# Kernel optimization log

Measured on AMD Instinct MI355X. Metric: run time of the kernel, lower is better.

Reference implementation:

```python
import jax, jax.numpy as jnp
import numpy as np
import math

B, NS, NT = 8, 512, 512
NSRC, NTRG = B * NS, B * NT
E = 32768
SCALAR_DIM, EMBED, ORI, LAYERS, K, KK = 20, 128, 1024, 3, 5, 25
CONV_IN = 2 * EMBED
FINAL_IN = ORI + LAYERS * EMBED


def sinusoidal_pos_emb(x):
    half = SCALAR_DIM // 2
    freqs = jnp.exp(-(math.log(10000.0) / (half - 1)) * jnp.arange(half, dtype=x.dtype))
    ang = x[:, None] * freqs[None, :]
    return jnp.concatenate([jnp.sin(ang), jnp.cos(ang)], axis=-1)


def spline_basis(pseudo):
    # open B-spline basis, degree 1, kernel_size K per dim, dim=2 (torch_spline_conv semantics)
    v = pseudo * (K - 1)
    lo = jnp.floor(v)
    frac = v - lo
    lo = lo.astype(jnp.int32)
    idxs, ws = [], []
    for s1 in (0, 1):
        for s0 in (0, 1):
            i0 = jnp.clip(lo[:, 0] + s0, 0, K - 1)
            i1 = jnp.clip(lo[:, 1] + s1, 0, K - 1)
            w0 = frac[:, 0] if s0 else 1.0 - frac[:, 0]
            w1 = frac[:, 1] if s1 else 1.0 - frac[:, 1]
            idxs.append(i0 + K * i1)
            ws.append(w0 * w1)
    idx = jnp.stack(idxs, 1)  # [E,4] kernel indices
    w = jnp.stack(ws, 1)      # [E,4] basis weights
    e = pseudo.shape[0]
    # dense [E,KK] coefficient matrix (<=4 nonzeros per row)
    return jnp.zeros((e, KK), pseudo.dtype).at[jnp.arange(e)[:, None], idx].add(w)


def spline_conv(x, edge_index, edge_attr, W, root, bias):
    # SplineConv(in=CONV_IN, out=EMBED, dim=2, kernel_size=5, degree=1, aggr='mean', root_weight=True)
    src, dst = edge_index[0], edge_index[1]
    x_j = x[src]                    # [E, in] gather of source features
    C = spline_basis(edge_attr)     # [E, KK]
    msg = jnp.zeros((x_j.shape[0], W.shape[-1]), x.dtype)
    for k in range(KK):             # fixed small kernel loop (25 GEMMs)
        msg = msg + (C[:, k:k + 1] * x_j) @ W[k]
    n = x.shape[0]
    agg = jax.ops.segment_sum(msg, dst, num_segments=n)
    deg = jax.ops.segment_sum(jnp.ones((msg.shape[0],), x.dtype), dst, num_segments=n)
    agg = agg / jnp.clip(deg, 1.0)[:, None]   # mean aggregation
    return agg + x @ root + bias


def masked_softmax(src, mask):
    out = jnp.where(mask, src, -jnp.inf)
    out = jax.nn.softmax(out, axis=-1)
    return jnp.where(mask, out, 0.0)


def setup_inputs() -> dict:
    key = jax.random.key(0)
    ks = jax.random.split(key, 16)
    s = 0.02
    # block-diagonal edges: both endpoints within the same graph
    gs = jax.random.randint(ks[11], (E,), 0, B)
    gt = jax.random.randint(ks[12], (E,), 0, B)
    ei_s = jnp.stack([gs * NS + jax.random.randint(ks[13], (E,), 0, NS),
                      gs * NS + jax.random.randint(ks[14], (E,), 0, NS)])
    ei_t = jnp.stack([gt * NT + jax.random.randint(ks[15], (E,), 0, NT),
                      gt * NT + jax.random.randint(ks[0], (E,), 0, NT)])
    return {
        "t": jax.random.uniform(ks[1], (B,)),
        "Xt": jax.random.uniform(ks[2], (B, NS, NT)),
        "x_s": jax.random.normal(ks[3], (NSRC, ORI)),
        "x_t": jax.random.normal(ks[4], (NTRG, ORI)),
        "ea_s": jax.random.uniform(ks[5], (E, 2)),
        "ea_t": jax.random.uniform(ks[6], (E, 2)),
        "lin0_w": jax.random.normal(ks[7], (ORI + 2 * SCALAR_DIM, EMBED)) * s,
        "lin0_b": jnp.zeros((EMBED,)),
        "lin_w": jax.random.normal(ks[8], (LAYERS - 1, EMBED + 2 * SCALAR_DIM, EMBED)) * s,
        "lin_b": jnp.zeros((LAYERS - 1, EMBED)),
        "conv_w": jax.random.normal(ks[9], (LAYERS, KK, CONV_IN, EMBED)) * s,
        "conv_root": jax.random.normal(ks[10], (LAYERS, CONV_IN, EMBED)) * s,
        "conv_bias": jnp.zeros((LAYERS, EMBED)),
        "final_w": jax.random.normal(jax.random.fold_in(key, 99), (FINAL_IN, EMBED)) * s,
        "final_b": jnp.zeros((EMBED,)),
        "ei_s": ei_s,
        "ei_t": ei_t,
        "s_mask": jnp.ones((B, NS), dtype=bool),
        "t_mask": jnp.ones((B, NT), dtype=bool),
        "mask_align": jnp.ones((B, NS, NT), dtype=bool),
    }


def reference(t, Xt, x_s, x_t, ea_s, ea_t, lin0_w, lin0_b, lin_w, lin_b,
              conv_w, conv_root, conv_bias, final_w, final_b,
              ei_s, ei_t, s_mask, t_mask, mask_align):
    # All graphs have exactly NS/NT nodes, so s_mask/t_mask are all-True:
    # boolean select x[s_mask] == reshape, and to_dense_batch == reshape.
    time_emb = sinusoidal_pos_emb(t)                                    # [B, 20]
    num_src = sinusoidal_pos_emb(Xt.sum(-1).reshape(-1) / 10.0)         # [NSRC, 20]
    num_trg = sinusoidal_pos_emb(jnp.swapaxes(Xt, 1, 2).sum(-1).reshape(-1) / 10.0)
    tf_src = jnp.repeat(time_emb, NS, axis=0)                           # per-node time features
    tf_trg = jnp.repeat(time_emb, NT, axis=0)
    xs_src, xs_trg = [x_s], [x_t]
    for i in range(LAYERS):
        w = lin0_w if i == 0 else lin_w[i - 1]
        b = lin0_b if i == 0 else lin_b[i - 1]
        xin_s = jnp.concatenate([xs_src[-1], num_src, tf_src], -1) @ w + b
        xin_t = jnp.concatenate([xs_trg[-1], num_trg, tf_trg], -1) @ w + b
        xp_s = xin_s.reshape(B, NS, EMBED)
        xp_t = xin_t.reshape(B, NT, EMBED)
        tgt_msg = jnp.einsum('bst,btd->bsd', Xt, xp_t)
        src_msg = jnp.einsum('bst,bsd->btd', Xt, xp_s)
        diff_s = (xp_s - tgt_msg).reshape(NSRC, EMBED)
        diff_t = (xp_t - src_msg).reshape(NTRG, EMBED)
        cat_s = jnp.concatenate([xin_s, diff_s], -1)
        cat_t = jnp.concatenate([xin_t, diff_t], -1)
        xs_src.append(jnp.tanh(spline_conv(cat_s, ei_s, ea_s, conv_w[i], conv_root[i], conv_bias[i])))
        xs_trg.append(jnp.tanh(spline_conv(cat_t, ei_t, ea_t, conv_w[i], conv_root[i], conv_bias[i])))
    h_s = jnp.concatenate(xs_src, -1) @ final_w + final_b
    h_t = jnp.concatenate(xs_trg, -1) @ final_w + final_b
    sim = jnp.einsum('bsd,btd->bst', h_s.reshape(B, NS, EMBED), h_t.reshape(B, NT, EMBED))
    return masked_softmax(sim, mask_align).reshape(NSRC, NT)
```

## Files before the change

### kernel.cpp

```cpp
#include <hip/hip_runtime.h>
#include <hip/hip_bf16.h>

typedef __hip_bfloat16 hb;
typedef short short8 __attribute__((ext_vector_type(8)));
typedef float f32x4 __attribute__((ext_vector_type(4)));
typedef unsigned short u16;

#define NNODE 4096
#define NEDGE 32768
#define EMB   128
#define ORI   1024
#define SD    20
#define CIN   256
#define NCV   3328
#define LDX   1088
#define LDS_  192

__device__ __forceinline__ float b2f(hb v){ return __bfloat162float(v); }
__device__ __forceinline__ hb f2b(float v){ return __float2bfloat16(v); }
__device__ __forceinline__ float u2f(u16 u){ hb h; __builtin_memcpy(&h, &u, 2); return b2f(h); }

__device__ __forceinline__ void split2(float x, u16& hi, u16& lo){
  hb h = f2b(x);
  float r = x - b2f(h);
  hb l = f2b(r);
  __builtin_memcpy(&hi, &h, 2);
  __builtin_memcpy(&lo, &l, 2);
}

__device__ __forceinline__ void gl16(const void* g, void* l){
  __builtin_amdgcn_global_load_lds(
      (const __attribute__((address_space(1))) unsigned int*)(size_t)g,
      (__attribute__((address_space(3))) unsigned int*)(unsigned int)(size_t)l,
      16, 0, 0);
}


__global__ __launch_bounds__(256) void k_rowsum(const float* __restrict__ Xt, float* __restrict__ rowsum){
  int row = blockIdx.x*4 + (threadIdx.x >> 6);
  int lane = threadIdx.x & 63;
  const float* p = Xt + (size_t)row*512;
  float s = 0.f;
  for (int i = lane; i < 512; i += 64) s += p[i];
  for (int off = 32; off; off >>= 1) s += __shfl_xor(s, off);
  if (lane == 0) rowsum[row] = s;
}

__global__ __launch_bounds__(256) void k_colsum(const float* __restrict__ Xt, float* __restrict__ colsum){
  int col = blockIdx.x*256 + threadIdx.x;
  int b = col >> 9, t = col & 511;
  const float* p = Xt + (size_t)b*512*512 + t;
  float s = 0.f;
  for (int sidx = 0; sidx < 512; ++sidx) s += p[(size_t)sidx*512];
  colsum[col] = s;
}

__global__ void k_posemb(const float* __restrict__ vals, int n, float scale, float* __restrict__ out){
  int i = blockIdx.x*blockDim.x + threadIdx.x;
  if (i >= n) return;
  float x = vals[i]*scale;
  float c = -logf(10000.f)/9.f;
  for (int j = 0; j < 10; ++j) {
    float f = expf(c*(float)j);
    out[i*20 + j]      = sinf(x*f);
    out[i*20 + 10 + j] = cosf(x*f);
  }
}

__global__ void k_basis2(const float* __restrict__ ea_s, const float* __restrict__ ea_t,
                         int* __restrict__ idx4, float* __restrict__ w4){
  int e = blockIdx.x*256 + threadIdx.x;
  const float* ea = (e < NEDGE) ? ea_s : ea_t;
  int el = e & (NEDGE-1);
  float p0 = ea[el*2]   * 4.0f;
  float p1 = ea[el*2+1] * 4.0f;
  float l0 = floorf(p0), l1 = floorf(p1);
  float f0 = p0 - l0, f1 = p1 - l1;
  int i0 = (int)l0, i1 = (int)l1;
  int j = 0;
  for (int s1 = 0; s1 <= 1; ++s1)
    for (int s0 = 0; s0 <= 1; ++s0) {
      int a  = min(max(i0 + s0, 0), 4);
      int bb = min(max(i1 + s1, 0), 4);
      float w = (s0 ? f0 : 1.f - f0) * (s1 ? f1 : 1.f - f1);
      idx4[e*4 + j] = a + 5*bb;
      w4[e*4 + j] = w;
      ++j;
    }
}

__global__ void k_count2(const int* __restrict__ ds, const int* __restrict__ dt, int* __restrict__ cnt){
  int e = blockIdx.x*256 + threadIdx.x;
  int side = e >= NEDGE;
  int el = e & (NEDGE-1);
  int node = (side ? dt : ds)[el];
  atomicAdd(&cnt[side*NNODE + node], 1);
}

__global__ __launch_bounds__(256) void k_scan2(const int* __restrict__ cntAll, int* __restrict__ rowptrAll,
                                               int* __restrict__ eposAll, float* __restrict__ invAll){
  int sideOff = blockIdx.x*NNODE;
  const int* cnt = cntAll + sideOff;
  int* rowptr = rowptrAll + blockIdx.x*(NNODE+1);
  int* epos = eposAll + sideOff;
  float* inv = invAll + sideOff;
  __shared__ int part[256];
  int tid = threadIdx.x;
  int base = tid*16;
  int v[16]; int s = 0;
  #pragma unroll
  for (int i = 0; i < 16; ++i){
    v[i] = s; int c = cnt[base+i]; s += c;
    inv[base+i] = 1.f / fmaxf((float)c, 1.f);
  }
  part[tid] = s; __syncthreads();
  int total = s;
  for (int off = 1; off < 256; off <<= 1){
    int y = (tid >= off) ? part[tid-off] : 0;
    __syncthreads();
    part[tid] += y;
    __syncthreads();
  }
  int excl = part[tid] - total;
  #pragma unroll
  for (int i = 0; i < 16; ++i){ int r = excl + v[i]; rowptr[base+i] = r; epos[base+i] = r; }
  if (tid == 255) rowptr[4096] = part[255];
}

__global__ void k_fill2(const int* __restrict__ ds, const int* __restrict__ dt,
                        int* __restrict__ eposAll, int* __restrict__ elistAll){
  int e = blockIdx.x*256 + threadIdx.x;
  int side = e >= NEDGE;
  int el = e & (NEDGE-1);
  int node = (side ? dt : ds)[el];
  int p = atomicAdd(&eposAll[side*NNODE + node], 1);
  elistAll[side*NEDGE + p] = el;
}

__global__ __launch_bounds__(256) void k_xtT2(const float* __restrict__ Xt,
    u16* __restrict__ XH, u16* __restrict__ XL, u16* __restrict__ TH, u16* __restrict__ TL){
  __shared__ float tile[64][65];
  int b = blockIdx.z, s0 = blockIdx.y*64, t0 = blockIdx.x*64;
  const float* src = Xt + (size_t)b*262144;
  size_t ob = (size_t)b*262144;
  #pragma unroll 4
  for (int p = 0; p < 16; ++p) {
    int idx = p*256 + threadIdx.x;
    int r = idx >> 6, c = idx & 63;
    float v = src[(size_t)(s0+r)*512 + t0 + c];
    tile[r][c] = v;
    size_t o = ob + (size_t)(s0+r)*512 + t0 + c;
    split2(v, XH[o], XL[o]);
  }
  __syncthreads();
  #pragma unroll 4
  for (int p = 0; p < 16; ++p) {
    int idx = p*256 + threadIdx.x;
    int r = idx >> 6, c = idx & 63;
    float v = tile[c][r];
    size_t o = ob + (size_t)(t0+r)*512 + s0 + c;
    split2(v, TH[o], TL[o]);
  }
}

__global__ void k_wT2(const float* __restrict__ src, u16* __restrict__ dH, u16* __restrict__ dL,
                      int Krows, int ldDst){
  int i = blockIdx.x*256 + threadIdx.x;
  if (i >= 128*ldDst) return;
  int n = i / ldDst, k = i - n*ldDst;
  float v = (k < Krows) ? src[(size_t)k*128 + n] : 0.f;
  split2(v, dH[i], dL[i]);
}

__global__ void k_wc2(const float* __restrict__ convw, const float* __restrict__ root,
                      u16* __restrict__ dH, u16* __restrict__ dL){
  int i = blockIdx.x*256 + threadIdx.x;
  int l = i / (NCV*CIN);
  int r = i - l*(NCV*CIN);
  int k = r & 255, n = r >> 8;
  const float* cw = convw + (size_t)l*25*CIN*128;
  const float* rt = root  + (size_t)l*CIN*128;
  float v;
  if (n < 3200) { int kk = n >> 7, col = n & 127; v = cw[((size_t)kk*256 + k)*128 + col]; }
  else          { int col = n & 127;              v = rt[(size_t)k*128 + col]; }
  split2(v, dH[i], dL[i]);
}

__global__ void k_aux2(const float* __restrict__ nums, const float* __restrict__ numt,
                       const float* __restrict__ temb,
                       u16* __restrict__ xH, u16* __restrict__ xL,
                       u16* __restrict__ xs0H, u16* __restrict__ xs0L,
                       u16* __restrict__ xs1H, u16* __restrict__ xs1L,
                       u16* __restrict__ xs2H, u16* __restrict__ xs2L){
  int i = blockIdx.x*256 + threadIdx.x;
  if (i >= 8192*64) return;
  int r = i >> 6, c = i & 63;
  int side = r >> 12, local = r & 4095, b = (r >> 9) & 7;
  float v = 0.f;
  if (c < 20) v = (side ? numt : nums)[local*20 + c];
  else if (c < 40) v = temb[b*20 + (c - 20)];
  u16 hi, lo; split2(v, hi, lo);
  size_t ox = (size_t)r*LDX + 1024 + c;
  xH[ox] = hi; xL[ox] = lo;
  size_t os = (size_t)r*LDS_ + 128 + c;
  xs0H[os] = hi; xs0L[os] = lo;
  xs1H[os] = hi; xs1L[os] = lo;
  xs2H[os] = hi; xs2L[os] = lo;
}

__global__ __launch_bounds__(256) void k_split(const float* __restrict__ src,
    u16* __restrict__ dH, u16* __restrict__ dL, int n){
  int i = blockIdx.x*256 + threadIdx.x;
  if (i < n) split2(src[i], dH[i], dL[i]);
}

__global__ __launch_bounds__(256) void k_splitW(const float* __restrict__ src,
    u16* __restrict__ dH, u16* __restrict__ dL, int srcW, int ldDst, long dstOff, int n){
  int i = blockIdx.x*256 + threadIdx.x;
  if (i >= n) return;
  int r = i / srcW, c = i - r*srcW;
  size_t o = (size_t)dstOff + (size_t)r*ldDst + c;
  split2(src[i], dH[o], dL[o]);
}

__global__ __launch_bounds__(256) void k_xinT(const float* __restrict__ src,
    u16* __restrict__ dH, u16* __restrict__ dL, float* __restrict__ cat){
  __shared__ float tile[64][65];
  int r0 = blockIdx.x*64, c0 = blockIdx.y*64;
  #pragma unroll 4
  for (int p = 0; p < 16; ++p) {
    int idx = p*256 + threadIdx.x;
    int r = idx >> 6, c = idx & 63;
    float v = src[(size_t)(r0+r)*128 + c0 + c];
    tile[r][c] = v;
    cat[(size_t)(r0+r)*256 + c0 + c]       = v;
    cat[(size_t)(r0+r)*256 + 128 + c0 + c] = v;
  }
  __syncthreads();
  #pragma unroll 4
  for (int p = 0; p < 16; ++p) {
    int idx = p*256 + threadIdx.x;
    int r = idx >> 6, c = idx & 63;
    float v = tile[c][r];
    size_t o = (size_t)(c0+r)*8192 + r0 + c;
    split2(v, dH[o], dL[o]);
  }
}

__global__ __launch_bounds__(256) void k_fillbias(const float* __restrict__ b, float* __restrict__ o){
  int i = blockIdx.x*256 + threadIdx.x;
  o[i] = b[i & 127];
}

__global__ __launch_bounds__(256) void k_gemm(
    const u16* __restrict__ Ah, const u16* __restrict__ Al, int lda, long aBatch,
    const u16* __restrict__ Bh, const u16* __restrict__ Bl, int ldb, long bBatch,
    int K, int flags, int ksplit,
    float* __restrict__ outF, const float* __restrict__ bias,
    int ldo, int oRowOff, int oBatchRows, const float* __restrict__ X,
    const u16* __restrict__ A2h, const u16* __restrict__ A2l,
    const u16* __restrict__ B2h, const u16* __restrict__ B2l, int oRowOff2)
{
  __shared__ __align__(16) u16 S[2][4][4096];
  const int tid = threadIdx.x;
  const int ln = tid & 63, w = tid >> 6;
  const int wm = (w >> 1)*64, wn = (w & 1)*64;
  const int l15 = ln & 15, q = ln >> 4;
  const int by = blockIdx.y;
  int bz = blockIdx.z;
  const u16* Aph = Ah; const u16* Apl = Al;
  const u16* Bph = Bh; const u16* Bpl = Bl;
  int rowOffSel = oRowOff;
  if (B2h != nullptr) {
    int half = gridDim.z >> 1;
    if (bz >= half) { bz -= half; Aph = A2h; Apl = A2l; Bph = B2h; Bpl = B2l; rowOffSel = oRowOff2; }
  }
  const int batch = bz / ksplit;
  const int kidx  = bz - batch*ksplit;
  const int bxm = blockIdx.x;
  const int kSteps = K >> 5;
  const int spc = (kSteps + ksplit - 1) / ksplit;
  const int kBeg = kidx * spc * 32;
  const int kEnd = min(K, kBeg + spc*32);
  if (kBeg >= kEnd) return;
  const u16* Abh = Aph + (size_t)batch*aBatch + (size_t)bxm*128*lda;
  const u16* Abl = Apl + (size_t)batch*aBatch + (size_t)bxm*128*lda;
  const u16* Bbh = Bph + (size_t)batch*bBatch + (size_t)by*128*ldb;
  const u16* Bbl = Bpl + (size_t)batch*bBatch + (size_t)by*128*ldb;

  f32x4 acc[4][4];
  #pragma unroll
  for (int i = 0; i < 4; ++i)
    #pragma unroll
    for (int j = 0; j < 4; ++j) acc[i][j] = (f32x4){0.f,0.f,0.f,0.f};

  const int r0 = w*32 + (ln >> 2);
  const int r1 = r0 + 16;
  const int c0 = ((ln & 3) ^ ((r0 >> 1) & 3)) * 8;
  const int c1 = ((ln & 3) ^ ((r1 >> 1) & 3)) * 8;

  auto stage = [&](int buf, int kc){
    char* wb = (char*)&S[buf][0][0] + w*2048;
    size_t gA0 = (size_t)r0*lda + kc + c0;
    size_t gA1 = (size_t)r1*lda + kc + c1;
    size_t gB0 = (size_t)r0*ldb + kc + c0;
    size_t gB1 = (size_t)r1*ldb + kc + c1;
    gl16(Abh + gA0, wb);           gl16(Abh + gA1, wb + 1024);
    gl16(Abl + gA0, wb + 8192);    gl16(Abl + gA1, wb + 9216);
    gl16(Bbh + gB0, wb + 16384);   gl16(Bbh + gB1, wb + 17408);
    gl16(Bbl + gB0, wb + 24576);   gl16(Bbl + gB1, wb + 25600);
  };

  auto compute = [&](int buf){
    const u16* AhS = &S[buf][0][0]; const u16* AlS = &S[buf][1][0];
    const u16* BhS = &S[buf][2][0]; const u16* BlS = &S[buf][3][0];
    short8 ah[4], al[4], bh[4], bl[4];
    #pragma unroll
    for (int i = 0; i < 4; ++i) {
      int ra = wm + i*16 + l15;
      int oa = ra*32 + ((q ^ ((ra >> 1) & 3)) << 3);
      ah[i] = *(const short8*)&AhS[oa];
      al[i] = *(const short8*)&AlS[oa];
      int rb = wn + i*16 + l15;
      int ob = rb*32 + ((q ^ ((rb >> 1) & 3)) << 3);
      bh[i] = *(const short8*)&BhS[ob];
      bl[i] = *(const short8*)&BlS[ob];
    }
    #pragma unroll
    for (int i = 0; i < 4; ++i)
      #pragma unroll
      for (int j = 0; j < 4; ++j) {
        acc[i][j] = __builtin_amdgcn_mfma_f32_16x16x32_bf16(ah[i], bl[j], acc[i][j], 0, 0, 0);
        acc[i][j] = __builtin_amdgcn_mfma_f32_16x16x32_bf16(al[i], bh[j], acc[i][j], 0, 0, 0);
        acc[i][j] = __builtin_amdgcn_mfma_f32_16x16x32_bf16(ah[i], bh[j], acc[i][j], 0, 0, 0);
      }
  };

  stage(0, kBeg);
  __syncthreads();
  int cur = 0;
  for (int kc = kBeg; kc < kEnd; kc += 32) {
    if (kc + 32 < kEnd) stage(cur ^ 1, kc + 32);
    compute(cur);
    __syncthreads();
    cur ^= 1;
  }

  const int rowBase = rowOffSel + batch*oBatchRows + bxm*128;
  #pragma unroll
  for (int i = 0; i < 4; ++i) {
    #pragma unroll
    for (int j = 0; j < 4; ++j) {
      int col = by*128 + wn + j*16 + l15;
      #pragma unroll
      for (int r = 0; r < 4; ++r) {
        int row = rowBase + wm + i*16 + q*4 + r;
        float v = acc[i][j][r];
        if (flags & 16) {
          hb hv = f2b(v);
          u16 uv; __builtin_memcpy(&uv, &hv, 2);
          ((u16*)outF)[(size_t)row*ldo + col] = uv;
        } else if (flags & 8) {
          if (flags & 4) unsafeAtomicAdd(&outF[(size_t)row*256 + 128 + col], -v);
          else           unsafeAtomicAdd(&outF[(size_t)row*ldo + col], v);
        } else {
          if (flags & 2) v += bias[col];
          if (flags & 1) v += outF[(size_t)row*ldo + col];
          if (flags & 4) {
            float xv = X[(size_t)row*128 + col];
            outF[(size_t)row*256 + col]       = xv;
            outF[(size_t)row*256 + 128 + col] = xv - v;
          } else {
            outF[(size_t)row*ldo + col] = v;
          }
        }
      }
    }
  }
}

__global__ __launch_bounds__(256) void k_aggtanh(const u16* __restrict__ Y,
    const int* __restrict__ src_s, const int* __restrict__ src_t,
    const int* __restrict__ elistAll, const int* __restrict__ rowptrAll,
    const int* __restrict__ idx4All, const float* __restrict__ w4All,
    const float* __restrict__ invAll, const float* __restrict__ biasAll, int layer,
    u16* __restrict__ xsH, u16* __restrict__ xsL){
  int n = blockIdx.x*2 + (threadIdx.x >> 7);
  int tid = threadIdx.x & 127;
  int side = n >> 12, local = n & 4095;
  const int* srcarr = side ? src_t : src_s;
  const int* elist  = elistAll + side*NEDGE;
  const int* rowptr = rowptrAll + side*(NNODE+1);
  const int* idx4   = idx4All + (size_t)side*NEDGE*4;
  const float* w4   = w4All + (size_t)side*NEDGE*4;
  const u16* Yb = Y + (size_t)side*NNODE*NCV;
  float acc = u2f(Yb[(size_t)local*NCV + 3200 + tid]);
  float wi = invAll[side*NNODE + local];
  int beg = rowptr[local], end = rowptr[local+1];
  for (int p = beg; p < end; ++p) {
    int e = elist[p];
    int sn = srcarr[e];
    const u16* yrow = Yb + (size_t)sn*NCV;
    #pragma unroll
    for (int j = 0; j < 4; ++j) {
      int k = idx4[e*4+j];
      float w = w4[e*4+j]*wi;
      acc += w * u2f(yrow[k*128 + tid]);
    }
  }
  float r = tanhf(acc + biasAll[layer*EMB + tid]);
  split2(r, xsH[(size_t)n*LDS_ + tid], xsL[(size_t)n*LDS_ + tid]);
}

__global__ __launch_bounds__(256) void k_softmax(const float* __restrict__ sim, float* __restrict__ out){
  int row = blockIdx.x, tid = threadIdx.x;
  __shared__ float red[8];
  float v0 = sim[(size_t)row*512 + tid];
  float v1 = sim[(size_t)row*512 + 256 + tid];
  int wid = tid >> 6, lane = tid & 63;
  float m = fmaxf(v0, v1);
  for (int off = 32; off; off >>= 1) m = fmaxf(m, __shfl_xor(m, off));
  if (lane == 0) red[wid] = m;
  __syncthreads();
  if (tid == 0) red[4] = fmaxf(fmaxf(red[0], red[1]), fmaxf(red[2], red[3]));
  __syncthreads();
  m = red[4];
  float e0 = expf(v0 - m), e1 = expf(v1 - m);
  float s = e0 + e1;
  for (int off = 32; off; off >>= 1) s += __shfl_xor(s, off);
  if (lane == 0) red[wid] = s;
  __syncthreads();
  if (tid == 0) red[5] = red[0] + red[1] + red[2] + red[3];
  __syncthreads();
  float inv = 1.f / red[5];
  out[(size_t)row*512 + tid]       = e0*inv;
  out[(size_t)row*512 + 256 + tid] = e1*inv;
}


extern "C" void kernel_launch(void* const* d_in, const int* in_sizes, int n_in,
                              void* d_out, int out_size, void* d_ws, size_t ws_size,
                              hipStream_t stream){
  (void)in_sizes; (void)n_in; (void)out_size; (void)ws_size;
  const float* t_in      = (const float*)d_in[0];
  const float* Xt        = (const float*)d_in[1];
  const float* x_s       = (const float*)d_in[2];
  const float* x_t       = (const float*)d_in[3];
  const float* ea_s      = (const float*)d_in[4];
  const float* ea_t      = (const float*)d_in[5];
  const float* lin0_w    = (const float*)d_in[6];
  const float* lin0_b    = (const float*)d_in[7];
  const float* lin_w     = (const float*)d_in[8];
  const float* lin_b     = (const float*)d_in[9];
  const float* conv_w    = (const float*)d_in[10];
  const float* conv_root = (const float*)d_in[11];
  const float* conv_bias = (const float*)d_in[12];
  const float* final_w   = (const float*)d_in[13];
  const float* final_b   = (const float*)d_in[14];
  const int*   ei_s      = (const int*)d_in[15];
  const int*   ei_t      = (const int*)d_in[16];
  float* out = (float*)d_out;

  char* wsb = (char*)d_ws;
  size_t off = 0;
  auto alloc = [&](size_t bytes)->char*{
    char* p = wsb + off;
    off += (bytes + 255) & ~(size_t)255;
    return p;
  };
  float* f_sums  = (float*)alloc(8192*4);
  float* f_temb  = (float*)alloc(8*SD*4);
  float* f_num   = (float*)alloc((size_t)8192*SD*4);
  int*   i_idx   = (int*)  alloc((size_t)2*NEDGE*4*4);
  float* f_w     = (float*)alloc((size_t)2*NEDGE*4*4);
  int*   i_cnt   = (int*)  alloc((size_t)2*NNODE*4);
  float* f_inv   = (float*)alloc((size_t)2*NNODE*4);
  int*   i_rp    = (int*)  alloc((size_t)2*(NNODE+1)*4);
  int*   i_ep    = (int*)  alloc((size_t)2*NNODE*4);
  int*   i_el    = (int*)  alloc((size_t)2*NEDGE*4);
  u16* XtH  = (u16*)alloc((size_t)8*512*512*2);
  u16* XtL  = (u16*)alloc((size_t)8*512*512*2);
  u16* XtTH = (u16*)alloc((size_t)8*512*512*2);
  u16* XtTL = (u16*)alloc((size_t)8*512*512*2);
  u16* w0H  = (u16*)alloc((size_t)128*1088*2);
  u16* w0L  = (u16*)alloc((size_t)128*1088*2);
  u16* w1H  = (u16*)alloc((size_t)128*192*2);
  u16* w1L  = (u16*)alloc((size_t)128*192*2);
  u16* w2H  = (u16*)alloc((size_t)128*192*2);
  u16* w2L  = (u16*)alloc((size_t)128*192*2);
  u16* wfH  = (u16*)alloc((size_t)128*1408*2);
  u16* wfL  = (u16*)alloc((size_t)128*1408*2);
  u16* wcH  = (u16*)alloc((size_t)3*NCV*CIN*2);
  u16* wcL  = (u16*)alloc((size_t)3*NCV*CIN*2);
  u16* xH   = (u16*)alloc((size_t)8192*LDX*2);
  u16* xL   = (u16*)alloc((size_t)8192*LDX*2);
  u16* xsH[3]; u16* xsL[3];
  for (int l = 0; l < 3; ++l) {
    xsH[l] = (u16*)alloc((size_t)8192*LDS_*2);
    xsL[l] = (u16*)alloc((size_t)8192*LDS_*2);
  }
  u16* catH = (u16*)alloc((size_t)8192*CIN*2);
  u16* catL = (u16*)alloc((size_t)8192*CIN*2);
  float* f_xin = (float*)alloc((size_t)8192*EMB*4);
  float* f_cat = (float*)alloc((size_t)8192*CIN*4);
  u16*   f_Y   = (u16*)  alloc((size_t)8192*NCV*2);
  float* f_sim = (float*)f_Y;
  u16* xiTH = (u16*)((char*)f_Y + (size_t)20*1024*1024);
  u16* xiTL = (u16*)((char*)f_Y + (size_t)23*1024*1024);
  u16* hH   = (u16*)((char*)f_Y + (size_t)26*1024*1024);
  u16* hL   = (u16*)((char*)f_Y + (size_t)29*1024*1024);

  auto gemm = [&](const u16* Ahp, const u16* Alp, int lda, long aB,
                  const u16* Bhp, const u16* Blp, int ldb, long bB,
                  int K, int flags, int ksplit, float* o, const float* bias,
                  int ldo, int rowOff, int oBR, const float* X, dim3 grid,
                  const u16* A2h = nullptr, const u16* A2l = nullptr,
                  const u16* B2h = nullptr, const u16* B2l = nullptr, int rowOff2 = 0){
    k_gemm<<<grid, 256, 0, stream>>>(Ahp, Alp, lda, aB, Bhp, Blp, ldb, bB, K, flags, ksplit,
                                     o, bias, ldo, rowOff, oBR, X,
                                     A2h, A2l, B2h, B2l, rowOff2);
  };

  k_xtT2<<<dim3(8,8,8), 256, 0, stream>>>(Xt, XtH, XtL, XtTH, XtTL);
  k_rowsum<<<NNODE/4, 256, 0, stream>>>(Xt, f_sums);
  k_colsum<<<NNODE/256, 256, 0, stream>>>(Xt, f_sums + NNODE);
  k_posemb<<<8192/256, 256, 0, stream>>>(f_sums, 8192, 0.1f, f_num);
  k_posemb<<<1, 64, 0, stream>>>(t_in, 8, 1.0f, f_temb);
  k_aux2<<<(8192*64)/256, 256, 0, stream>>>(f_num, f_num + (size_t)NNODE*SD, f_temb,
      xH, xL, xsH[0], xsL[0], xsH[1], xsL[1], xsH[2], xsL[2]);
  k_basis2<<<2*NEDGE/256, 256, 0, stream>>>(ea_s, ea_t, i_idx, f_w);
  hipMemsetAsync(i_cnt, 0, 2*NNODE*4, stream);
  k_count2<<<2*NEDGE/256, 256, 0, stream>>>(ei_s + NEDGE, ei_t + NEDGE, i_cnt);
  k_scan2<<<2, 256, 0, stream>>>(i_cnt, i_rp, i_ep, f_inv);
  k_fill2<<<2*NEDGE/256, 256, 0, stream>>>(ei_s + NEDGE, ei_t + NEDGE, i_ep, i_el);
  k_wT2<<<(128*1088)/256, 256, 0, stream>>>(lin0_w, w0H, w0L, 1064, 1088);
  k_wT2<<<(128*192)/256, 256, 0, stream>>>(lin_w, w1H, w1L, 168, 192);
  k_wT2<<<(128*192)/256, 256, 0, stream>>>(lin_w + (size_t)168*128, w2H, w2L, 168, 192);
  k_wT2<<<(128*1408)/256, 256, 0, stream>>>(final_w, wfH, wfL, 1408, 1408);
  k_wc2<<<(3*NCV*CIN)/256, 256, 0, stream>>>(conv_w, conv_root, wcH, wcL);
  k_splitW<<<(4096*1024)/256, 256, 0, stream>>>(x_s, xH, xL, 1024, LDX, 0, 4096*1024);
  k_splitW<<<(4096*1024)/256, 256, 0, stream>>>(x_t, xH, xL, 1024, LDX, (long)4096*LDX, 4096*1024);

  for (int i = 0; i < 3; ++i) {
    const u16* wTh = (i == 0) ? w0H : (i == 1) ? w1H : w2H;
    const u16* wTl = (i == 0) ? w0L : (i == 1) ? w1L : w2L;
    const float* bv = (i == 0) ? lin0_b : lin_b + (i-1)*EMB;
    int ldw = (i == 0) ? 1088 : 192;

    k_fillbias<<<4096, 256, 0, stream>>>(bv, f_xin);
    const u16* A0h = (i == 0) ? xH : xsH[i-1];
    const u16* A0l = (i == 0) ? xL : xsL[i-1];
    int lda = (i == 0) ? LDX : LDS_;
    int Kf  = (i == 0) ? LDX : LDS_;
    int ks  = (i == 0) ? 8 : 6;
    gemm(A0h, A0l, lda, 0, wTh, wTl, ldw, 0,
         Kf, 8, ks, f_xin, nullptr, EMB, 0, 0, nullptr, dim3(64,1,ks));

    k_xinT<<<dim3(128,2), 256, 0, stream>>>(f_xin, xiTH, xiTL, f_cat);
    gemm(XtH, XtL, 512, 262144, xiTH + 4096, xiTL + 4096, 8192, 512,
         512, 4|8, 8, f_cat, nullptr, 256, 0, 512, nullptr, dim3(4,1,128),
         XtTH, XtTL, xiTH, xiTL, NNODE);
    k_split<<<(8192*CIN)/256, 256, 0, stream>>>(f_cat, catH, catL, 8192*CIN);

    gemm(catH, catL, CIN, 0,
         wcH + (size_t)i*NCV*CIN, wcL + (size_t)i*NCV*CIN, CIN, 0,
         CIN, 16, 1, (float*)f_Y, nullptr, NCV, 0, 0, nullptr, dim3(32,26,2),
         catH + (size_t)NNODE*CIN, catL + (size_t)NNODE*CIN,
         wcH + (size_t)i*NCV*CIN, wcL + (size_t)i*NCV*CIN, NNODE);
    k_aggtanh<<<4096, 256, 0, stream>>>(f_Y, ei_s, ei_t, i_el, i_rp,
        i_idx, f_w, f_inv, conv_bias, i, xsH[i], xsL[i]);
  }

  float* f_h = f_xin;
  k_fillbias<<<4096, 256, 0, stream>>>(final_b, f_h);
  gemm(xH, xL, LDX, 0, wfH, wfL, 1408, 0,
       1024, 8, 8, f_h, nullptr, EMB, 0, 0, nullptr, dim3(64,1,8));
  for (int l = 0; l < 3; ++l)
    gemm(xsH[l], xsL[l], LDS_, 0, wfH + 1024 + l*128, wfL + 1024 + l*128, 1408, 0,
         128, 8, 4, f_h, nullptr, EMB, 0, 0, nullptr, dim3(64,1,4));
  k_split<<<(8192*EMB)/256, 256, 0, stream>>>(f_h, hH, hL, 8192*EMB);

  hipMemsetAsync(f_sim, 0, (size_t)4096*512*4, stream);
  gemm(hH, hL, EMB, 65536, hH + (size_t)4096*EMB, hL + (size_t)4096*EMB, EMB, 65536,
       EMB, 8, 4, f_sim, nullptr, 512, 0, 512, nullptr, dim3(4,4,32));

  k_softmax<<<NNODE, 256, 0, stream>>>(f_sim, out);
}
```

Measured before the change: 840.1 us.

## Fuse setup kernels and merge per-layer final GEMMs into one wide GEMM

```diff
diff --git a/kernel.cpp b/kernel.cpp
--- a/kernel.cpp
+++ b/kernel.cpp
@@ -14,7 +14,7 @@
 #define CIN   256
 #define NCV   3328
 #define LDX   1088
-#define LDS_  192
+#define XSW   576
 
 __device__ __forceinline__ float b2f(hb v){ return __bfloat162float(v); }
 __device__ __forceinline__ hb f2b(float v){ return __float2bfloat16(v); }
@@ -35,43 +35,37 @@
       16, 0, 0);
 }
 
-
-__global__ __launch_bounds__(256) void k_rowsum(const float* __restrict__ Xt, float* __restrict__ rowsum){
-  int row = blockIdx.x*4 + (threadIdx.x >> 6);
-  int lane = threadIdx.x & 63;
-  const float* p = Xt + (size_t)row*512;
-  float s = 0.f;
-  for (int i = lane; i < 512; i += 64) s += p[i];
-  for (int off = 32; off; off >>= 1) s += __shfl_xor(s, off);
-  if (lane == 0) rowsum[row] = s;
-}
-
-__global__ __launch_bounds__(256) void k_colsum(const float* __restrict__ Xt, float* __restrict__ colsum){
-  int col = blockIdx.x*256 + threadIdx.x;
-  int b = col >> 9, t = col & 511;
-  const float* p = Xt + (size_t)b*512*512 + t;
-  float s = 0.f;
-  for (int sidx = 0; sidx < 512; ++sidx) s += p[(size_t)sidx*512];
-  colsum[col] = s;
-}
-
-__global__ void k_posemb(const float* __restrict__ vals, int n, float scale, float* __restrict__ out){
-  int i = blockIdx.x*blockDim.x + threadIdx.x;
-  if (i >= n) return;
-  float x = vals[i]*scale;
-  float c = -logf(10000.f)/9.f;
-  for (int j = 0; j < 10; ++j) {
-    float f = expf(c*(float)j);
-    out[i*20 + j]      = sinf(x*f);
-    out[i*20 + 10 + j] = cosf(x*f);
-  }
-}
-
-__global__ void k_basis2(const float* __restrict__ ea_s, const float* __restrict__ ea_t,
-                         int* __restrict__ idx4, float* __restrict__ w4){
+__device__ __forceinline__ float pefreq(int j){
+  return expf((-logf(10000.f)/9.f)*(float)j);
+}
+
+
+__global__ __launch_bounds__(256) void k_rc(const float* __restrict__ Xt, float* __restrict__ sums){
+  if (blockIdx.x < 1024) {
+    int row = blockIdx.x*4 + (threadIdx.x >> 6);
+    int lane = threadIdx.x & 63;
+    const float* p = Xt + (size_t)row*512;
+    float s = 0.f;
+    for (int i = lane; i < 512; i += 64) s += p[i];
+    for (int off = 32; off; off >>= 1) s += __shfl_xor(s, off);
+    if (lane == 0) sums[row] = s;
+  } else {
+    int col = (blockIdx.x - 1024)*256 + threadIdx.x;
+    int b = col >> 9, t = col & 511;
+    const float* p = Xt + (size_t)b*512*512 + t;
+    float s = 0.f;
+    for (int sidx = 0; sidx < 512; ++sidx) s += p[(size_t)sidx*512];
+    sums[NNODE + col] = s;
+  }
+}
+
+__global__ void k_bc(const float* __restrict__ ea_s, const float* __restrict__ ea_t,
+                     const int* __restrict__ ds, const int* __restrict__ dt,
+                     int* __restrict__ idx4, float* __restrict__ w4, int* __restrict__ cnt){
   int e = blockIdx.x*256 + threadIdx.x;
-  const float* ea = (e < NEDGE) ? ea_s : ea_t;
+  int side = e >= NEDGE;
   int el = e & (NEDGE-1);
+  const float* ea = side ? ea_t : ea_s;
   float p0 = ea[el*2]   * 4.0f;
   float p1 = ea[el*2+1] * 4.0f;
   float l0 = floorf(p0), l1 = floorf(p1);
@@ -87,12 +81,6 @@
       w4[e*4 + j] = w;
       ++j;
     }
-}
-
-__global__ void k_count2(const int* __restrict__ ds, const int* __restrict__ dt, int* __restrict__ cnt){
-  int e = blockIdx.x*256 + threadIdx.x;
-  int side = e >= NEDGE;
-  int el = e & (NEDGE-1);
   int node = (side ? dt : ds)[el];
   atomicAdd(&cnt[side*NNODE + node], 1);
 }
@@ -163,13 +151,43 @@
   }
 }
 
-__global__ void k_wT2(const float* __restrict__ src, u16* __restrict__ dH, u16* __restrict__ dL,
-                      int Krows, int ldDst){
+#define SEG0 139264
+#define SEG1 163840
+#define SEG2 188416
+#define SEG3 368640
+#define SEG4 442368
+__global__ __launch_bounds__(256) void k_wprep(const float* __restrict__ lin0_w,
+    const float* __restrict__ lin_w, const float* __restrict__ final_w,
+    u16* __restrict__ w0H, u16* __restrict__ w0L,
+    u16* __restrict__ w1H, u16* __restrict__ w1L,
+    u16* __restrict__ w2H, u16* __restrict__ w2L,
+    u16* __restrict__ wfH, u16* __restrict__ wfL,
+    u16* __restrict__ wf3H, u16* __restrict__ wf3L){
   int i = blockIdx.x*256 + threadIdx.x;
-  if (i >= 128*ldDst) return;
-  int n = i / ldDst, k = i - n*ldDst;
-  float v = (k < Krows) ? src[(size_t)k*128 + n] : 0.f;
-  split2(v, dH[i], dL[i]);
+  float v; u16 *dH, *dL; int e;
+  if (i < SEG0) {
+    e = i; int n = e/1088, k = e - n*1088;
+    v = (k < 1064) ? lin0_w[(size_t)k*128 + n] : 0.f;
+    dH = w0H; dL = w0L;
+  } else if (i < SEG1) {
+    e = i - SEG0; int n = e/192, k = e - n*192;
+    v = (k < 168) ? lin_w[(size_t)k*128 + n] : 0.f;
+    dH = w1H; dL = w1L;
+  } else if (i < SEG2) {
+    e = i - SEG1; int n = e/192, k = e - n*192;
+    v = (k < 168) ? lin_w[(size_t)(168 + k)*128 + n] : 0.f;
+    dH = w2H; dL = w2L;
+  } else if (i < SEG3) {
+    e = i - SEG2; int n = e/1408, k = e - n*1408;
+    v = final_w[(size_t)k*128 + n];
+    dH = wfH; dL = wfL;
+  } else {
+    e = i - SEG3; int n = e/576, k = e - n*576;
+    int l = k/192, kk = k - l*192;
+    v = (kk < 128) ? final_w[(size_t)(1024 + l*128 + kk)*128 + n] : 0.f;
+    dH = wf3H; dL = wf3L;
+  }
+  split2(v, dH[e], dL[e]);
 }
 
 __global__ void k_wc2(const float* __restrict__ convw, const float* __restrict__ root,
@@ -186,26 +204,30 @@
   split2(v, dH[i], dL[i]);
 }
 
-__global__ void k_aux2(const float* __restrict__ nums, const float* __restrict__ numt,
-                       const float* __restrict__ temb,
+__global__ void k_aux2(const float* __restrict__ sums, const float* __restrict__ t_in,
                        u16* __restrict__ xH, u16* __restrict__ xL,
-                       u16* __restrict__ xs0H, u16* __restrict__ xs0L,
-                       u16* __restrict__ xs1H, u16* __restrict__ xs1L,
-                       u16* __restrict__ xs2H, u16* __restrict__ xs2L){
+                       u16* __restrict__ xsAllH, u16* __restrict__ xsAllL){
   int i = blockIdx.x*256 + threadIdx.x;
   if (i >= 8192*64) return;
   int r = i >> 6, c = i & 63;
   int side = r >> 12, local = r & 4095, b = (r >> 9) & 7;
   float v = 0.f;
-  if (c < 20) v = (side ? numt : nums)[local*20 + c];
-  else if (c < 40) v = temb[b*20 + (c - 20)];
+  if (c < 20) {
+    float x = sums[side*NNODE + local] * 0.1f;
+    v = (c < 10) ? sinf(x*pefreq(c)) : cosf(x*pefreq(c-10));
+  } else if (c < 40) {
+    float x = t_in[b];
+    int cc = c - 20;
+    v = (cc < 10) ? sinf(x*pefreq(cc)) : cosf(x*pefreq(cc-10));
+  }
   u16 hi, lo; split2(v, hi, lo);
   size_t ox = (size_t)r*LDX + 1024 + c;
   xH[ox] = hi; xL[ox] = lo;
-  size_t os = (size_t)r*LDS_ + 128 + c;
-  xs0H[os] = hi; xs0L[os] = lo;
-  xs1H[os] = hi; xs1L[os] = lo;
-  xs2H[os] = hi; xs2L[os] = lo;
+  #pragma unroll
+  for (int l = 0; l < 3; ++l) {
+    size_t os = (size_t)r*XSW + l*192 + 128 + c;
+    xsAllH[os] = hi; xsAllL[os] = lo;
+  }
 }
 
 __global__ __launch_bounds__(256) void k_split(const float* __restrict__ src,
@@ -266,8 +288,7 @@
   const int ln = tid & 63, w = tid >> 6;
   const int wm = (w >> 1)*64, wn = (w & 1)*64;
   const int l15 = ln & 15, q = ln >> 4;
-  const int by = blockIdx.y;
-  int bz = blockIdx.z;
+  int bxm = blockIdx.x, by = blockIdx.y, bz = blockIdx.z;
   const u16* Aph = Ah; const u16* Apl = Al;
   const u16* Bph = Bh; const u16* Bpl = Bl;
   int rowOffSel = oRowOff;
@@ -277,7 +298,6 @@
   }
   const int batch = bz / ksplit;
   const int kidx  = bz - batch*ksplit;
-  const int bxm = blockIdx.x;
   const int kSteps = K >> 5;
   const int spc = (kSteps + ksplit - 1) / ksplit;
   const int kBeg = kidx * spc * 32;
@@ -409,7 +429,7 @@
     }
   }
   float r = tanhf(acc + biasAll[layer*EMB + tid]);
-  split2(r, xsH[(size_t)n*LDS_ + tid], xsL[(size_t)n*LDS_ + tid]);
+  split2(r, xsH[(size_t)n*XSW + tid], xsL[(size_t)n*XSW + tid]);
 }
 
 __global__ __launch_bounds__(256) void k_softmax(const float* __restrict__ sim, float* __restrict__ out){
@@ -469,8 +489,6 @@
     return p;
   };
   float* f_sums  = (float*)alloc(8192*4);
-  float* f_temb  = (float*)alloc(8*SD*4);
-  float* f_num   = (float*)alloc((size_t)8192*SD*4);
   int*   i_idx   = (int*)  alloc((size_t)2*NEDGE*4*4);
   float* f_w     = (float*)alloc((size_t)2*NEDGE*4*4);
   int*   i_cnt   = (int*)  alloc((size_t)2*NNODE*4);
@@ -490,15 +508,14 @@
   u16* w2L  = (u16*)alloc((size_t)128*192*2);
   u16* wfH  = (u16*)alloc((size_t)128*1408*2);
   u16* wfL  = (u16*)alloc((size_t)128*1408*2);
+  u16* wf3H = (u16*)alloc((size_t)128*576*2);
+  u16* wf3L = (u16*)alloc((size_t)128*576*2);
   u16* wcH  = (u16*)alloc((size_t)3*NCV*CIN*2);
   u16* wcL  = (u16*)alloc((size_t)3*NCV*CIN*2);
   u16* xH   = (u16*)alloc((size_t)8192*LDX*2);
   u16* xL   = (u16*)alloc((size_t)8192*LDX*2);
-  u16* xsH[3]; u16* xsL[3];
-  for (int l = 0; l < 3; ++l) {
-    xsH[l] = (u16*)alloc((size_t)8192*LDS_*2);
-    xsL[l] = (u16*)alloc((size_t)8192*LDS_*2);
-  }
+  u16* xsAllH = (u16*)alloc((size_t)8192*XSW*2);
+  u16* xsAllL = (u16*)alloc((size_t)8192*XSW*2);
   u16* catH = (u16*)alloc((size_t)8192*CIN*2);
   u16* catL = (u16*)alloc((size_t)8192*CIN*2);
   float* f_xin = (float*)alloc((size_t)8192*EMB*4);
@@ -522,21 +539,15 @@
   };
 
   k_xtT2<<<dim3(8,8,8), 256, 0, stream>>>(Xt, XtH, XtL, XtTH, XtTL);
-  k_rowsum<<<NNODE/4, 256, 0, stream>>>(Xt, f_sums);
-  k_colsum<<<NNODE/256, 256, 0, stream>>>(Xt, f_sums + NNODE);
-  k_posemb<<<8192/256, 256, 0, stream>>>(f_sums, 8192, 0.1f, f_num);
-  k_posemb<<<1, 64, 0, stream>>>(t_in, 8, 1.0f, f_temb);
-  k_aux2<<<(8192*64)/256, 256, 0, stream>>>(f_num, f_num + (size_t)NNODE*SD, f_temb,
-      xH, xL, xsH[0], xsL[0], xsH[1], xsL[1], xsH[2], xsL[2]);
-  k_basis2<<<2*NEDGE/256, 256, 0, stream>>>(ea_s, ea_t, i_idx, f_w);
+  k_rc<<<1040, 256, 0, stream>>>(Xt, f_sums);
+  k_aux2<<<(8192*64)/256, 256, 0, stream>>>(f_sums, t_in, xH, xL, xsAllH, xsAllL);
   hipMemsetAsync(i_cnt, 0, 2*NNODE*4, stream);
-  k_count2<<<2*NEDGE/256, 256, 0, stream>>>(ei_s + NEDGE, ei_t + NEDGE, i_cnt);
+  k_bc<<<2*NEDGE/256, 256, 0, stream>>>(ea_s, ea_t, ei_s + NEDGE, ei_t + NEDGE,
+                                        i_idx, f_w, i_cnt);
   k_scan2<<<2, 256, 0, stream>>>(i_cnt, i_rp, i_ep, f_inv);
   k_fill2<<<2*NEDGE/256, 256, 0, stream>>>(ei_s + NEDGE, ei_t + NEDGE, i_ep, i_el);
-  k_wT2<<<(128*1088)/256, 256, 0, stream>>>(lin0_w, w0H, w0L, 1064, 1088);
-  k_wT2<<<(128*192)/256, 256, 0, stream>>>(lin_w, w1H, w1L, 168, 192);
-  k_wT2<<<(128*192)/256, 256, 0, stream>>>(lin_w + (size_t)168*128, w2H, w2L, 168, 192);
-  k_wT2<<<(128*1408)/256, 256, 0, stream>>>(final_w, wfH, wfL, 1408, 1408);
+  k_wprep<<<SEG4/256, 256, 0, stream>>>(lin0_w, lin_w, final_w,
+      w0H, w0L, w1H, w1L, w2H, w2L, wfH, wfL, wf3H, wf3L);
   k_wc2<<<(3*NCV*CIN)/256, 256, 0, stream>>>(conv_w, conv_root, wcH, wcL);
   k_splitW<<<(4096*1024)/256, 256, 0, stream>>>(x_s, xH, xL, 1024, LDX, 0, 4096*1024);
   k_splitW<<<(4096*1024)/256, 256, 0, stream>>>(x_t, xH, xL, 1024, LDX, (long)4096*LDX, 4096*1024);
@@ -548,10 +559,10 @@
     int ldw = (i == 0) ? 1088 : 192;
 
     k_fillbias<<<4096, 256, 0, stream>>>(bv, f_xin);
-    const u16* A0h = (i == 0) ? xH : xsH[i-1];
-    const u16* A0l = (i == 0) ? xL : xsL[i-1];
-    int lda = (i == 0) ? LDX : LDS_;
-    int Kf  = (i == 0) ? LDX : LDS_;
+    const u16* A0h = (i == 0) ? xH : xsAllH + (i-1)*192;
+    const u16* A0l = (i == 0) ? xL : xsAllL + (i-1)*192;
+    int lda = (i == 0) ? LDX : XSW;
+    int Kf  = (i == 0) ? LDX : 192;
     int ks  = (i == 0) ? 8 : 6;
     gemm(A0h, A0l, lda, 0, wTh, wTl, ldw, 0,
          Kf, 8, ks, f_xin, nullptr, EMB, 0, 0, nullptr, dim3(64,1,ks));
@@ -568,16 +579,15 @@
          catH + (size_t)NNODE*CIN, catL + (size_t)NNODE*CIN,
          wcH + (size_t)i*NCV*CIN, wcL + (size_t)i*NCV*CIN, NNODE);
     k_aggtanh<<<4096, 256, 0, stream>>>(f_Y, ei_s, ei_t, i_el, i_rp,
-        i_idx, f_w, f_inv, conv_bias, i, xsH[i], xsL[i]);
+        i_idx, f_w, f_inv, conv_bias, i, xsAllH + i*192, xsAllL + i*192);
   }
 
   float* f_h = f_xin;
   k_fillbias<<<4096, 256, 0, stream>>>(final_b, f_h);
   gemm(xH, xL, LDX, 0, wfH, wfL, 1408, 0,
        1024, 8, 8, f_h, nullptr, EMB, 0, 0, nullptr, dim3(64,1,8));
-  for (int l = 0; l < 3; ++l)
-    gemm(xsH[l], xsL[l], LDS_, 0, wfH + 1024 + l*128, wfL + 1024 + l*128, 1408, 0,
-         128, 8, 4, f_h, nullptr, EMB, 0, 0, nullptr, dim3(64,1,4));
+  gemm(xsAllH, xsAllL, XSW, 0, wf3H, wf3L, 576, 0,
+       576, 8, 6, f_h, nullptr, EMB, 0, 0, nullptr, dim3(64,1,6));
   k_split<<<(8192*EMB)/256, 256, 0, stream>>>(f_h, hH, hL, 8192*EMB);
 
   hipMemsetAsync(f_sim, 0, (size_t)4096*512*4, stream);
```

New measurement: 785.9 us. 6.5% less time.
